# Optimization experiments

Hardware: AMD Instinct MI355X
Metric: run time of the kernel (lower is better)

The kernel has to match this reference:

```python
import jax, jax.numpy as jnp
import numpy as np

B, T, I, H = 64, 2048, 128, 256


def setup_inputs() -> dict:
    key = jax.random.key(0)
    k1, k2, k3 = jax.random.split(key, 3)
    inputs = jax.random.normal(k1, (B, T, I), dtype=jnp.float32)
    # 4 gates (input, forget, context, output), each an affine op on [x_t, h]
    W_x = jax.random.normal(k2, (4, I, H), dtype=jnp.float32) * (1.0 / np.sqrt(I))
    W_h = jax.random.normal(k3, (4, H, H), dtype=jnp.float32) * (1.0 / np.sqrt(H))
    b = jnp.zeros((4, H), dtype=jnp.float32)
    return {"inputs": inputs, "W_x": W_x, "W_h": W_h, "b": b}


def reference(inputs, W_x, W_h, b):
    # inputs: [B, T, I]; W_x: [4, I, H]; W_h: [4, H, H]; b: [4, H]
    Bb = inputs.shape[0]
    Hh = W_h.shape[-1]
    h0 = jnp.zeros((Bb, Hh), dtype=inputs.dtype)
    c0 = jnp.zeros((Bb, Hh), dtype=inputs.dtype)

    def step(carry, x_t):
        h, c = carry
        # all 4 gate pre-activations at once: [4, B, H]
        g = (jnp.einsum('bi,gih->gbh', x_t, W_x)
             + jnp.einsum('bh,ghk->gbk', h, W_h)
             + b[:, None, :])
        i_gate = jax.nn.sigmoid(g[0])
        f_gate = jax.nn.sigmoid(g[1])
        g_gate = jnp.tanh(g[2])
        o_gate = jax.nn.sigmoid(g[3])
        c_new = f_gate * c + i_gate * g_gate
        h_new = o_gate * jnp.tanh(c_new)
        return (h_new, c_new), h_new

    xs = jnp.swapaxes(inputs, 0, 1)  # [T, B, I]
    (_, _), hs = jax.lax.scan(step, (h0, c0), xs)  # hs: [T, B, H]
    return jnp.swapaxes(hs, 0, 1)  # [B, T, H]
```

## Files before the change

### kernel.cpp

```cpp
#include <hip/hip_runtime.h>
#include <hip/hip_bf16.h>


#define B_ 64
#define T_ 2048
#define I_ 128
#define H_ 256
#define NC 1024

typedef __attribute__((ext_vector_type(8))) short bf16x8;
typedef __attribute__((ext_vector_type(4))) float f32x4;

static __device__ __forceinline__ unsigned short f2bf(float f) {
    unsigned u = __builtin_bit_cast(unsigned, f);
    u = (u + 0x7FFFu + ((u >> 16) & 1u)) >> 16;
    return (unsigned short)u;
}

static __device__ __forceinline__ int dot4(unsigned a, unsigned b, int c) {
#if __has_builtin(__builtin_amdgcn_sdot4)
    return __builtin_amdgcn_sdot4((int)a, (int)b, c, false);
#else
    int r = c;
    r += (int)(signed char)(a) * (int)(signed char)(b);
    r += (int)(signed char)(a >> 8) * (int)(signed char)(b >> 8);
    r += (int)(signed char)(a >> 16) * (int)(signed char)(b >> 16);
    r += (int)(signed char)(a >> 24) * (int)(signed char)(b >> 24);
    return r;
#endif
}

__global__ void pack_wh(const float* __restrict__ Wh, unsigned* __restrict__ wq,
                        float* __restrict__ sws) {
    int col = blockIdx.x;
    int g = col >> 8, j = col & 255;
    int lane = threadIdx.x;
    float v[4];
    float m = 0.f;
#pragma unroll
    for (int u = 0; u < 4; ++u) {
        int k = lane * 4 + u;
        v[u] = Wh[(g * H_ + k) * H_ + j];
        m = fmaxf(m, fabsf(v[u]));
    }
#pragma unroll
    for (int off = 32; off; off >>= 1) m = fmaxf(m, __shfl_xor(m, off));
    float mm = (m > 0.f) ? m : 1.f;
    float inv = 127.f / mm;
    unsigned pack = 0;
#pragma unroll
    for (int u = 0; u < 4; ++u) {
        int q = (int)rintf(v[u] * inv);
        q = max(-127, min(127, q));
        pack |= ((unsigned)(q & 255)) << (8 * u);
    }
    wq[col * 64 + lane] = pack;
    if (lane == 0) sws[col] = mm / (127.f * 127.f);
}

__global__ void pack_wx(const float* __restrict__ Wx,
                        unsigned short* __restrict__ bxp) {
    int f = blockIdx.x * blockDim.x + threadIdx.x;
    int j = f & 7;
    int col = (f >> 3) & 1023;
    int c16 = f >> 13;
    int k = (c16 >> 2) * 32 + (c16 & 3) * 8 + j;
    int g = col >> 8, h = col & 255;
    bxp[f] = f2bf(Wx[(g * I_ + k) * H_ + h]);
}

__global__ __launch_bounds__(256) void gemm_gx(
    const float* __restrict__ A, const unsigned short* __restrict__ Bp,
    unsigned short* __restrict__ Cg) {
    __shared__ uint4 sm[4096];
    int tid = threadIdx.x;
    int mt = blockIdx.x, nt = blockIdx.y;

    const float* Ab = A + (size_t)mt * 128 * I_;
    unsigned* dstA = (unsigned*)sm;
#pragma unroll
    for (int it = 0; it < 16; ++it) {
        int flat = it * 1024 + tid * 4;
        float4 a4 = *(const float4*)(Ab + flat);
        int m = flat >> 7, k0 = flat & 127;
        int c16 = k0 >> 3, j0 = k0 & 7;
        unsigned lo = (unsigned)f2bf(a4.x) | ((unsigned)f2bf(a4.y) << 16);
        unsigned hi = (unsigned)f2bf(a4.z) | ((unsigned)f2bf(a4.w) << 16);
        int didx = ((c16 * 128 + m) * 16 + j0 * 2) >> 2;
        dstA[didx] = lo;
        dstA[didx + 1] = hi;
    }
    const uint4* Bq = (const uint4*)Bp;
#pragma unroll
    for (int it = 0; it < 8; ++it) {
        int chunk = it * 2 + (tid >> 7);
        int inner = tid & 127;
        sm[2048 + chunk * 128 + inner] = Bq[chunk * 1024 + nt * 128 + inner];
    }
    __syncthreads();

    int wid = tid >> 6, lane = tid & 63;
    int r = lane & 15, q = lane >> 4;
    int mw = (wid & 1) * 64, nw = (wid >> 1) * 64;
    f32x4 acc[4][4] = {};
#pragma unroll
    for (int ki = 0; ki < 4; ++ki) {
        bf16x8 af[4], bfr[4];
#pragma unroll
        for (int x = 0; x < 4; ++x) {
            af[x] = __builtin_bit_cast(bf16x8,
                                       sm[(ki * 4 + q) * 128 + mw + x * 16 + r]);
            bfr[x] = __builtin_bit_cast(
                bf16x8, sm[2048 + (ki * 4 + q) * 128 + nw + x * 16 + r]);
        }
#pragma unroll
        for (int x = 0; x < 4; ++x)
#pragma unroll
            for (int y = 0; y < 4; ++y)
                acc[x][y] = __builtin_amdgcn_mfma_f32_16x16x32_bf16(
                    af[x], bfr[y], acc[x][y], 0, 0, 0);
    }
    __syncthreads();

    _Float16* ct = (_Float16*)sm;
#pragma unroll
    for (int x = 0; x < 4; ++x)
#pragma unroll
        for (int y = 0; y < 4; ++y)
#pragma unroll
            for (int g2 = 0; g2 < 4; ++g2) {
                int row = mw + x * 16 + q * 4 + g2;
                int colc = nw + y * 16 + r;
                ct[row * 128 + colc] = (_Float16)acc[x][y][g2];
            }
    __syncthreads();
    int m = tid >> 1, half = tid & 1;
    const uint4* src = (const uint4*)sm;
    uint4* dstg =
        (uint4*)(Cg + ((size_t)(mt * 128 + m) * NC + nt * 128 + half * 64));
#pragma unroll
    for (int i = 0; i < 8; ++i) dstg[i] = src[m * 16 + half * 8 + i];
}

#define DOTQ(acc, hv, wv)            \
    acc = dot4(hv.x, wv.x, acc);     \
    acc = dot4(hv.y, wv.y, acc);     \
    acc = dot4(hv.z, wv.z, acc);     \
    acc = dot4(hv.w, wv.w, acc);

__global__ __launch_bounds__(512) void lstm_rec(
    const unsigned short* __restrict__ gx, const uint4* __restrict__ wq4,
    const float* __restrict__ sws, const float* __restrict__ bias,
    float* __restrict__ out) {
    int b = blockIdx.x, tid = threadIdx.x;
    int col0 = tid, col1 = tid + 512;

    uint4 w0[16], w1[16];
#pragma unroll
    for (int i = 0; i < 16; ++i) {
        w0[i] = wq4[col0 * 16 + i];
        w1[i] = wq4[col1 * 16 + i];
    }
    float s0 = sws[col0], s1 = sws[col1];
    float bb0 = bias[col0], bb1 = bias[col1];

    __shared__ uint4 hq[2][16];
    __shared__ float p1buf[256];
    if (tid < 64) ((unsigned*)&hq[0][0])[tid] = 0u;
    __syncthreads();

    float c = 0.f;
    const _Float16* gxh = (const _Float16*)gx;
    size_t rowbase = (size_t)b * T_;
    float gx0 = (float)gxh[rowbase * NC + col0];
    float gx1 = (float)gxh[rowbase * NC + col1];

    for (int t = 0; t < T_; ++t) {
        size_t row = rowbase + t;
        float nx0 = (float)gxh[(row + 1) * NC + col0];
        float nx1 = (float)gxh[(row + 1) * NC + col1];

        int a0 = 0, a1 = 0, a2 = 0, a3 = 0;
        const uint4* hb = hq[t & 1];
#pragma unroll
        for (int i = 0; i < 16; i += 2) {
            uint4 h0v = hb[i], h1v = hb[i + 1];
            DOTQ(a0, h0v, w0[i]);
            DOTQ(a2, h0v, w1[i]);
            DOTQ(a1, h1v, w0[i + 1]);
            DOTQ(a3, h1v, w1[i + 1]);
        }
        float g0 = (float)(a0 + a1) * s0 + gx0 + bb0;
        float g1 = (float)(a2 + a3) * s1 + gx1 + bb1;

        float r0 = 1.f / (1.f + __expf(-g0));
        float r1;
        if (tid < 256) {
            float e = __expf(-2.f * g1);
            r1 = 2.f / (1.f + e) - 1.f;
            p1buf[tid] = r0 * r1;
        } else {
            r1 = 1.f / (1.f + __expf(-g1));
        }
        __syncthreads();
        if (tid >= 256) {
            int j = tid - 256;
            c = r0 * c + p1buf[j];
            float e = __expf(-2.f * c);
            float th = 2.f / (1.f + e) - 1.f;
            float h = r1 * th;
            out[row * H_ + j] = h;
            int qv = (int)rintf(h * 127.f);
            ((signed char*)hq[(t + 1) & 1])[j] = (signed char)qv;
        }
        __syncthreads();
        gx0 = nx0;
        gx1 = nx1;
    }
}

extern "C" void kernel_launch(void* const* d_in, const int* in_sizes, int n_in,
                              void* d_out, int out_size, void* d_ws,
                              size_t ws_size, hipStream_t stream) {
    const float* inputs = (const float*)d_in[0];
    const float* Wx = (const float*)d_in[1];
    const float* Wh = (const float*)d_in[2];
    const float* bias = (const float*)d_in[3];
    float* out = (float*)d_out;

    char* ws = (char*)d_ws;
    unsigned short* gxbuf = (unsigned short*)ws;
    size_t off = (size_t)B_ * T_ * NC * 2;
    unsigned* wq = (unsigned*)(ws + off);
    off += (size_t)NC * 64 * 4;
    float* sws = (float*)(ws + off);
    off += (size_t)NC * 4;
    unsigned short* bxp = (unsigned short*)(ws + off);
    off += (size_t)I_ * NC * 2;

    pack_wh<<<NC, 64, 0, stream>>>(Wh, wq, sws);
    pack_wx<<<(I_ * NC) / 256, 256, 0, stream>>>(Wx, bxp);
    gemm_gx<<<dim3((B_ * T_) / 128, NC / 128), 256, 0, stream>>>(inputs, bxp,
                                                                 gxbuf);
    lstm_rec<<<B_, 512, 0, stream>>>(gxbuf, (const uint4*)wq, sws, bias, out);
}
```

Before: 2.327 ms.

## Give each LSTM thread all four gates of one hidden unit, dropping a barrier

The recurrent kernel now runs 256 threads per batch row, and each thread holds the int8 weights for all four gates of one hidden unit (256 VGPRs of weights). The cell update therefore happens entirely in registers, which removes the shared p1buf exchange and one of the two __syncthreads per timestep. Gate nonlinearities use the hardware reciprocal instead of a division. In exchange each thread does twice the dot-product work on half as many waves. The heavy register pressure risks spilling, and the lower wave count gives less latency hiding.

```diff
diff --git a/kernel.cpp b/kernel.cpp
--- a/kernel.cpp
+++ b/kernel.cpp
@@ -30,6 +30,10 @@
 #endif
 }
 
+static __device__ __forceinline__ float fastrcp(float x) {
+    return __builtin_amdgcn_rcpf(x);
+}
+
 __global__ void pack_wh(const float* __restrict__ Wh, unsigned* __restrict__ wq,
                         float* __restrict__ sws) {
     int col = blockIdx.x;
@@ -142,80 +146,89 @@
     for (int i = 0; i < 8; ++i) dstg[i] = src[m * 16 + half * 8 + i];
 }
 
-#define DOTQ(acc, hv, wv)            \
-    acc = dot4(hv.x, wv.x, acc);     \
-    acc = dot4(hv.y, wv.y, acc);     \
-    acc = dot4(hv.z, wv.z, acc);     \
-    acc = dot4(hv.w, wv.w, acc);
-
-__global__ __launch_bounds__(512) void lstm_rec(
+__global__ __launch_bounds__(256, 1) void lstm_rec(
     const unsigned short* __restrict__ gx, const uint4* __restrict__ wq4,
     const float* __restrict__ sws, const float* __restrict__ bias,
     float* __restrict__ out) {
-    int b = blockIdx.x, tid = threadIdx.x;
-    int col0 = tid, col1 = tid + 512;
-
-    uint4 w0[16], w1[16];
+    int b = blockIdx.x, j = threadIdx.x;
+
+    uint4 w0[16], w1[16], w2[16], w3[16];
 #pragma unroll
     for (int i = 0; i < 16; ++i) {
-        w0[i] = wq4[col0 * 16 + i];
-        w1[i] = wq4[col1 * 16 + i];
-    }
-    float s0 = sws[col0], s1 = sws[col1];
-    float bb0 = bias[col0], bb1 = bias[col1];
+        w0[i] = wq4[(0 * H_ + j) * 16 + i];
+        w1[i] = wq4[(1 * H_ + j) * 16 + i];
+        w2[i] = wq4[(2 * H_ + j) * 16 + i];
+        w3[i] = wq4[(3 * H_ + j) * 16 + i];
+    }
+    float s0 = sws[0 * H_ + j], s1 = sws[1 * H_ + j];
+    float s2 = sws[2 * H_ + j], s3 = sws[3 * H_ + j];
+    float b0 = bias[0 * H_ + j], b1 = bias[1 * H_ + j];
+    float b2 = bias[2 * H_ + j], b3 = bias[3 * H_ + j];
 
     __shared__ uint4 hq[2][16];
-    __shared__ float p1buf[256];
-    if (tid < 64) ((unsigned*)&hq[0][0])[tid] = 0u;
+    if (j < 16) hq[0][j] = (uint4){0u, 0u, 0u, 0u};
     __syncthreads();
 
     float c = 0.f;
     const _Float16* gxh = (const _Float16*)gx;
     size_t rowbase = (size_t)b * T_;
-    float gx0 = (float)gxh[rowbase * NC + col0];
-    float gx1 = (float)gxh[rowbase * NC + col1];
+    float gv0 = (float)gxh[rowbase * NC + 0 * H_ + j];
+    float gv1 = (float)gxh[rowbase * NC + 1 * H_ + j];
+    float gv2 = (float)gxh[rowbase * NC + 2 * H_ + j];
+    float gv3 = (float)gxh[rowbase * NC + 3 * H_ + j];
 
     for (int t = 0; t < T_; ++t) {
         size_t row = rowbase + t;
-        float nx0 = (float)gxh[(row + 1) * NC + col0];
-        float nx1 = (float)gxh[(row + 1) * NC + col1];
-
+        size_t prow = rowbase + ((t < T_ - 1) ? (t + 1) : t);
+        float nv0 = (float)gxh[prow * NC + 0 * H_ + j];
+        float nv1 = (float)gxh[prow * NC + 1 * H_ + j];
+        float nv2 = (float)gxh[prow * NC + 2 * H_ + j];
+        float nv3 = (float)gxh[prow * NC + 3 * H_ + j];
+
+        const uint4* hb = hq[t & 1];
         int a0 = 0, a1 = 0, a2 = 0, a3 = 0;
-        const uint4* hb = hq[t & 1];
+        int e0 = 0, e1 = 0, e2 = 0, e3 = 0;
 #pragma unroll
         for (int i = 0; i < 16; i += 2) {
-            uint4 h0v = hb[i], h1v = hb[i + 1];
-            DOTQ(a0, h0v, w0[i]);
-            DOTQ(a2, h0v, w1[i]);
-            DOTQ(a1, h1v, w0[i + 1]);
-            DOTQ(a3, h1v, w1[i + 1]);
+            uint4 h0 = hb[i], h1 = hb[i + 1];
+            a0 = dot4(w0[i].x, h0.x, a0); a0 = dot4(w0[i].y, h0.y, a0);
+            a0 = dot4(w0[i].z, h0.z, a0); a0 = dot4(w0[i].w, h0.w, a0);
+            a1 = dot4(w1[i].x, h0.x, a1); a1 = dot4(w1[i].y, h0.y, a1);
+            a1 = dot4(w1[i].z, h0.z, a1); a1 = dot4(w1[i].w, h0.w, a1);
+            a2 = dot4(w2[i].x, h0.x, a2); a2 = dot4(w2[i].y, h0.y, a2);
+            a2 = dot4(w2[i].z, h0.z, a2); a2 = dot4(w2[i].w, h0.w, a2);
+            a3 = dot4(w3[i].x, h0.x, a3); a3 = dot4(w3[i].y, h0.y, a3);
+            a3 = dot4(w3[i].z, h0.z, a3); a3 = dot4(w3[i].w, h0.w, a3);
+            e0 = dot4(w0[i + 1].x, h1.x, e0); e0 = dot4(w0[i + 1].y, h1.y, e0);
+            e0 = dot4(w0[i + 1].z, h1.z, e0); e0 = dot4(w0[i + 1].w, h1.w, e0);
+            e1 = dot4(w1[i + 1].x, h1.x, e1); e1 = dot4(w1[i + 1].y, h1.y, e1);
+            e1 = dot4(w1[i + 1].z, h1.z, e1); e1 = dot4(w1[i + 1].w, h1.w, e1);
+            e2 = dot4(w2[i + 1].x, h1.x, e2); e2 = dot4(w2[i + 1].y, h1.y, e2);
+            e2 = dot4(w2[i + 1].z, h1.z, e2); e2 = dot4(w2[i + 1].w, h1.w, e2);
+            e3 = dot4(w3[i + 1].x, h1.x, e3); e3 = dot4(w3[i + 1].y, h1.y, e3);
+            e3 = dot4(w3[i + 1].z, h1.z, e3); e3 = dot4(w3[i + 1].w, h1.w, e3);
         }
-        float g0 = (float)(a0 + a1) * s0 + gx0 + bb0;
-        float g1 = (float)(a2 + a3) * s1 + gx1 + bb1;
-
-        float r0 = 1.f / (1.f + __expf(-g0));
-        float r1;
-        if (tid < 256) {
-            float e = __expf(-2.f * g1);
-            r1 = 2.f / (1.f + e) - 1.f;
-            p1buf[tid] = r0 * r1;
-        } else {
-            r1 = 1.f / (1.f + __expf(-g1));
-        }
+        float g0 = (float)(a0 + e0) * s0 + gv0 + b0;
+        float g1 = (float)(a1 + e1) * s1 + gv1 + b1;
+        float g2 = (float)(a2 + e2) * s2 + gv2 + b2;
+        float g3 = (float)(a3 + e3) * s3 + gv3 + b3;
+
+        float ig = fastrcp(1.f + __expf(-g0));
+        float fg = fastrcp(1.f + __expf(-g1));
+        float eg = __expf(-2.f * g2);
+        float gg = 2.f * fastrcp(1.f + eg) - 1.f;
+        float og = fastrcp(1.f + __expf(-g3));
+
+        c = fg * c + ig * gg;
+        float ec = __expf(-2.f * c);
+        float th = 2.f * fastrcp(1.f + ec) - 1.f;
+        float h = og * th;
+        out[row * H_ + j] = h;
+        int qv = (int)rintf(h * 127.f);
+        ((signed char*)hq[(t + 1) & 1])[j] = (signed char)qv;
         __syncthreads();
-        if (tid >= 256) {
-            int j = tid - 256;
-            c = r0 * c + p1buf[j];
-            float e = __expf(-2.f * c);
-            float th = 2.f / (1.f + e) - 1.f;
-            float h = r1 * th;
-            out[row * H_ + j] = h;
-            int qv = (int)rintf(h * 127.f);
-            ((signed char*)hq[(t + 1) & 1])[j] = (signed char)qv;
-        }
-        __syncthreads();
-        gx0 = nx0;
-        gx1 = nx1;
+
+        gv0 = nv0; gv1 = nv1; gv2 = nv2; gv3 = nv3;
     }
 }
 
@@ -242,5 +255,5 @@
     pack_wx<<<(I_ * NC) / 256, 256, 0, stream>>>(Wx, bxp);
     gemm_gx<<<dim3((B_ * T_) / 128, NC / 128), 256, 0, stream>>>(inputs, bxp,
                                                                  gxbuf);
-    lstm_rec<<<B_, 512, 0, stream>>>(gxbuf, (const uint4*)wq, sws, bias, out);
-}
+    lstm_rec<<<B_, 256, 0, stream>>>(gxbuf, (const uint4*)wq, sws, bias, out);
+}
```

Result: slower. 3.232 ms (+38.9%).

## Use one thread per gate column with warp shuffles to drop a barrier

Applied to the files above, without the earlier changes.

The recurrent kernel now runs 1024 threads per block, one per gate column. Each wave holds 16 hidden units across all four gates, so the gate combination uses __shfl inside the wave instead of a shared-memory exchange. This removes one __syncthreads per timestep and halves the per-thread register weight footprint. It also switches divisions to hardware reciprocal and clamps the gx prefetch at the last step. Cost: four times more threads active only in the activation phase, plus a 1024-thread block-wide barrier.

```diff
diff --git a/kernel.cpp b/kernel.cpp
--- a/kernel.cpp
+++ b/kernel.cpp
@@ -30,6 +30,10 @@
 #endif
 }
 
+static __device__ __forceinline__ float fastrcp(float x) {
+    return __builtin_amdgcn_rcpf(x);
+}
+
 __global__ void pack_wh(const float* __restrict__ Wh, unsigned* __restrict__ wq,
                         float* __restrict__ sws) {
     int col = blockIdx.x;
@@ -142,80 +146,79 @@
     for (int i = 0; i < 8; ++i) dstg[i] = src[m * 16 + half * 8 + i];
 }
 
-#define DOTQ(acc, hv, wv)            \
-    acc = dot4(hv.x, wv.x, acc);     \
-    acc = dot4(hv.y, wv.y, acc);     \
-    acc = dot4(hv.z, wv.z, acc);     \
-    acc = dot4(hv.w, wv.w, acc);
-
-__global__ __launch_bounds__(512) void lstm_rec(
+__global__ __launch_bounds__(1024, 4) void lstm_rec(
     const unsigned short* __restrict__ gx, const uint4* __restrict__ wq4,
     const float* __restrict__ sws, const float* __restrict__ bias,
     float* __restrict__ out) {
     int b = blockIdx.x, tid = threadIdx.x;
-    int col0 = tid, col1 = tid + 512;
-
-    uint4 w0[16], w1[16];
-#pragma unroll
-    for (int i = 0; i < 16; ++i) {
-        w0[i] = wq4[col0 * 16 + i];
-        w1[i] = wq4[col1 * 16 + i];
-    }
-    float s0 = sws[col0], s1 = sws[col1];
-    float bb0 = bias[col0], bb1 = bias[col1];
+    int w = tid >> 6;
+    int lane = tid & 63;
+    int g = lane >> 4;
+    int jj = lane & 15;
+    int j = w * 16 + jj;
+    int col = g * H_ + j;
+
+    uint4 wv[16];
+#pragma unroll
+    for (int i = 0; i < 16; ++i) wv[i] = wq4[col * 16 + i];
+    float sc = sws[col];
+    float bb = bias[col];
 
     __shared__ uint4 hq[2][16];
-    __shared__ float p1buf[256];
-    if (tid < 64) ((unsigned*)&hq[0][0])[tid] = 0u;
+    if (tid < 16) hq[0][tid] = (uint4){0u, 0u, 0u, 0u};
     __syncthreads();
 
     float c = 0.f;
     const _Float16* gxh = (const _Float16*)gx;
     size_t rowbase = (size_t)b * T_;
-    float gx0 = (float)gxh[rowbase * NC + col0];
-    float gx1 = (float)gxh[rowbase * NC + col1];
+    float gxv = (float)gxh[rowbase * NC + col];
 
     for (int t = 0; t < T_; ++t) {
         size_t row = rowbase + t;
-        float nx0 = (float)gxh[(row + 1) * NC + col0];
-        float nx1 = (float)gxh[(row + 1) * NC + col1];
-
+        size_t prow = rowbase + ((t < T_ - 1) ? (t + 1) : t);
+        float nxv = (float)gxh[prow * NC + col];
+
+        const uint4* hb = hq[t & 1];
         int a0 = 0, a1 = 0, a2 = 0, a3 = 0;
-        const uint4* hb = hq[t & 1];
-#pragma unroll
-        for (int i = 0; i < 16; i += 2) {
-            uint4 h0v = hb[i], h1v = hb[i + 1];
-            DOTQ(a0, h0v, w0[i]);
-            DOTQ(a2, h0v, w1[i]);
-            DOTQ(a1, h1v, w0[i + 1]);
-            DOTQ(a3, h1v, w1[i + 1]);
+#pragma unroll
+        for (int ib = 0; ib < 4; ++ib) {
+            uint4 h0 = hb[ib * 4 + 0], h1 = hb[ib * 4 + 1];
+            uint4 h2 = hb[ib * 4 + 2], h3 = hb[ib * 4 + 3];
+            uint4 w0 = wv[ib * 4 + 0], w1 = wv[ib * 4 + 1];
+            uint4 w2 = wv[ib * 4 + 2], w3 = wv[ib * 4 + 3];
+            a0 = dot4(w0.x, h0.x, a0); a0 = dot4(w0.y, h0.y, a0);
+            a0 = dot4(w0.z, h0.z, a0); a0 = dot4(w0.w, h0.w, a0);
+            a1 = dot4(w1.x, h1.x, a1); a1 = dot4(w1.y, h1.y, a1);
+            a1 = dot4(w1.z, h1.z, a1); a1 = dot4(w1.w, h1.w, a1);
+            a2 = dot4(w2.x, h2.x, a2); a2 = dot4(w2.y, h2.y, a2);
+            a2 = dot4(w2.z, h2.z, a2); a2 = dot4(w2.w, h2.w, a2);
+            a3 = dot4(w3.x, h3.x, a3); a3 = dot4(w3.y, h3.y, a3);
+            a3 = dot4(w3.z, h3.z, a3); a3 = dot4(w3.w, h3.w, a3);
         }
-        float g0 = (float)(a0 + a1) * s0 + gx0 + bb0;
-        float g1 = (float)(a2 + a3) * s1 + gx1 + bb1;
-
-        float r0 = 1.f / (1.f + __expf(-g0));
-        float r1;
-        if (tid < 256) {
-            float e = __expf(-2.f * g1);
-            r1 = 2.f / (1.f + e) - 1.f;
-            p1buf[tid] = r0 * r1;
-        } else {
-            r1 = 1.f / (1.f + __expf(-g1));
-        }
-        __syncthreads();
-        if (tid >= 256) {
-            int j = tid - 256;
-            c = r0 * c + p1buf[j];
-            float e = __expf(-2.f * c);
-            float th = 2.f / (1.f + e) - 1.f;
-            float h = r1 * th;
+        float gpre = (float)((a0 + a1) + (a2 + a3)) * sc + gxv + bb;
+
+        bool isg = (g == 2);
+        float arg = isg ? (-2.f * gpre) : (-gpre);
+        float e = __expf(arg);
+        float r = fastrcp(1.f + e);
+        float v = isg ? (2.f * r - 1.f) : r;
+
+        float fv = __shfl(v, jj + 16, 64);
+        float gv = __shfl(v, jj + 32, 64);
+        float ov = __shfl(v, jj + 48, 64);
+
+        if (g == 0) {
+            c = fv * c + v * gv;
+            float ec = __expf(-2.f * c);
+            float th = 2.f * fastrcp(1.f + ec) - 1.f;
+            float h = ov * th;
             out[row * H_ + j] = h;
             int qv = (int)rintf(h * 127.f);
             ((signed char*)hq[(t + 1) & 1])[j] = (signed char)qv;
         }
         __syncthreads();
-        gx0 = nx0;
-        gx1 = nx1;
+
+        gxv = nxv;
     }
 }
 
@@ -242,5 +245,5 @@
     pack_wx<<<(I_ * NC) / 256, 256, 0, stream>>>(Wx, bxp);
     gemm_gx<<<dim3((B_ * T_) / 128, NC / 128), 256, 0, stream>>>(inputs, bxp,
                                                                  gxbuf);
-    lstm_rec<<<B_, 512, 0, stream>>>(gxbuf, (const uint4*)wq, sws, bias, out);
-}
+    lstm_rec<<<B_, 1024, 0, stream>>>(gxbuf, (const uint4*)wq, sws, bias, out);
+}
```

Measured after the change: 2.292 ms. About the same (-1.5%).
